# Performance work log

Hardware: AMD Instinct MI355X
Metric: run time of the kernel (lower is better)

The kernel has to match this reference:

```python
import jax, jax.numpy as jnp
import numpy as np
from jax import lax

B, C, H, W = 16, 256, 64, 64
EXP = 2
C2 = C * EXP  # expanded channels
EPS = 1e-5


def setup_inputs() -> dict:
    key = jax.random.key(0)
    ks = jax.random.split(key, 8)
    def he(k, shape, fan_out):
        return jax.random.normal(k, shape, jnp.float32) * np.sqrt(2.0 / fan_out)
    return {
        "f": jax.random.normal(ks[0], (B, C, H, W), jnp.float32),
        "ln_gamma": jnp.ones((C,), jnp.float32),
        "ln_beta": jnp.zeros((C,), jnp.float32),
        "w_expand": he(ks[1], (C2, C), C2),          # 1x1 conv [out,in]
        "freq_real": jnp.ones((C2,), jnp.float32),
        "freq_imag": jnp.zeros((C2,), jnp.float32),
        "w_poly": he(ks[2], (C2, C2), C2),
        "w_dw": he(ks[3], (C2, 1, 3, 3), 9),          # depthwise 3x3, fan_out=1*3*3
        "w_pw": he(ks[4], (C2, C2), C2),
        "w_final": he(ks[5], (C, C2), C),
    }


def reference(f, ln_gamma, ln_beta, w_expand, freq_real, freq_imag,
              w_poly, w_dw, w_pw, w_final):
    # LayerNorm over channel dim (torch permutes to NHWC, norms last dim)
    mu = jnp.mean(f, axis=1, keepdims=True)
    var = jnp.var(f, axis=1, keepdims=True)
    f1 = (f - mu) * lax.rsqrt(var + EPS)
    f1 = f1 * ln_gamma[None, :, None, None] + ln_beta[None, :, None, None]
    # 1x1 expand
    f2 = jnp.einsum('bchw,oc->bohw', f1, w_expand)
    # FFT2 -> multiply by per-channel complex scalar (r + i*j) -> IFFT2 -> real.
    # Since the filter is constant over all frequencies and f2 is real, this is
    # exactly Re((r+i*j) * f2) = r * f2; freq_imag contributes nothing.
    f4 = f2 * freq_real[None, :, None, None]
    # polymerize 1x1
    f5 = jnp.einsum('bchw,oc->bohw', f4, w_poly)
    # depthwise 3x3, SAME padding
    f6 = lax.conv_general_dilated(
        f5, w_dw, window_strides=(1, 1), padding='SAME',
        dimension_numbers=('NCHW', 'OIHW', 'NCHW'), feature_group_count=C2)
    # pointwise 1x1
    f6 = jnp.einsum('bchw,oc->bohw', f6, w_pw)
    # GELU (exact erf, torch default) gating
    f7 = jax.nn.gelu(f6, approximate=False) * f6
    # 1x1 reduce + residual
    f8 = jnp.einsum('bchw,oc->bohw', f7, w_final)
    return f + f8
```

## Files before the change

### kernel.cpp

```cpp
#include <hip/hip_runtime.h>
#include <hip/hip_bf16.h>
#include <math.h>

#define Bn 16
#define Cc 256
#define Hh 64
#define Ww 64
#define HW 4096
#define C2 512
#define Pp 65536
#define EPSc 1e-5f

typedef __attribute__((ext_vector_type(8))) short short8;
typedef __attribute__((ext_vector_type(4))) float floatx4;

__global__ __launch_bounds__(256)
void combine_weights(const float* __restrict__ w_expand,
                     const float* __restrict__ freq_real,
                     const float* __restrict__ w_poly,
                     const float* __restrict__ gamma,
                     const float* __restrict__ beta,
                     __hip_bfloat16* __restrict__ W1g_b,
                     float* __restrict__ bias1,
                     float* __restrict__ wsum) {
    int o = blockIdx.x;
    int c = threadIdx.x;
    float acc = 0.f;
    const float* wp = w_poly + (size_t)o * C2;
    for (int m = 0; m < C2; ++m) {
        acc += wp[m] * freq_real[m] * w_expand[(size_t)m * Cc + c];
    }
    float wg = acc * gamma[c];
    W1g_b[(size_t)o * Cc + c] = __float2bfloat16(wg);
    __shared__ float redB[256];
    __shared__ float redG[256];
    redB[c] = acc * beta[c];
    redG[c] = wg;
    __syncthreads();
    for (int s = 128; s > 0; s >>= 1) {
        if (c < s) { redB[c] += redB[c + s]; redG[c] += redG[c + s]; }
        __syncthreads();
    }
    if (c == 0) { bias1[o] = redB[0]; wsum[o] = redG[0]; }
}

__global__ __launch_bounds__(256)
void to_bf16(const float* __restrict__ a, __hip_bfloat16* __restrict__ o, int n) {
    int i = (blockIdx.x * 256 + threadIdx.x) * 4;
    if (i < n) {
        float4 v = *(const float4*)&a[i];
        __hip_bfloat16 r[4];
        r[0] = __float2bfloat16(v.x);
        r[1] = __float2bfloat16(v.y);
        r[2] = __float2bfloat16(v.z);
        r[3] = __float2bfloat16(v.w);
        *(uint2*)&o[i] = *(const uint2*)r;
    }
}

__global__ __launch_bounds__(256)
void pad_dw(const float* __restrict__ w_dw, float* __restrict__ w_dw_p) {
    int i = blockIdx.x * 256 + threadIdx.x;
    if (i < C2 * 12) {
        int k = i / 12, j = i - k * 12;
        w_dw_p[i] = (j < 9) ? w_dw[k * 9 + j] : 0.f;
    }
}

#define XPAD 264

__global__ __launch_bounds__(512, 4)
void gemm1f(const float* __restrict__ f,
            const __hip_bfloat16* __restrict__ W1g_b,
            const float* __restrict__ bias1,
            const float* __restrict__ wsum,
            __hip_bfloat16* __restrict__ f5) {
    __shared__ __hip_bfloat16 As[64 * XPAD];
    __shared__ float redS[32 * 64];
    __shared__ float redQ[32 * 64];
    __shared__ float muS[64];
    __shared__ float rsS[64];

    int flat = blockIdx.x;
    int b = flat >> 6;
    int h = flat & 63;
    int s0 = h * 64;

    int tid = threadIdx.x;
    int x = tid & 15;
    int cg = tid >> 4;

    const float* fb = f + (size_t)b * Cc * HW + s0 + x * 4;
    unsigned* Asu = (unsigned*)&As[0];

    float lsum[4] = {0.f, 0.f, 0.f, 0.f};
    float lsq[4]  = {0.f, 0.f, 0.f, 0.f};
#pragma unroll
    for (int i = 0; i < 4; ++i) {
        int cp = i * 32 + cg;
        float4 v0 = *(const float4*)&fb[(size_t)(cp * 2) * HW];
        float4 v1 = *(const float4*)&fb[(size_t)(cp * 2 + 1) * HW];
        float a0[4] = {v0.x, v0.y, v0.z, v0.w};
        float a1[4] = {v1.x, v1.y, v1.z, v1.w};
#pragma unroll
        for (int j = 0; j < 4; ++j) {
            lsum[j] += a0[j] + a1[j];
            lsq[j]  += a0[j] * a0[j] + a1[j] * a1[j];
            unsigned pk = ((unsigned)__bfloat16_as_ushort(__float2bfloat16(a1[j])) << 16)
                        |  (unsigned)__bfloat16_as_ushort(__float2bfloat16(a0[j]));
            Asu[(size_t)(x * 4 + j) * (XPAD / 2) + cp] = pk;
        }
    }
#pragma unroll
    for (int j = 0; j < 4; ++j) {
        redS[cg * 64 + x * 4 + j] = lsum[j];
        redQ[cg * 64 + x * 4 + j] = lsq[j];
    }

    int lane = tid & 63, wave = tid >> 6;
    int col = lane & 15, quad = lane >> 4;
    int c0w = wave * 64;
    const __hip_bfloat16* Bp = W1g_b + (size_t)(c0w + col) * Cc + quad * 8;
    short8 b_cur[4], b_nxt[4];
#pragma unroll
    for (int j = 0; j < 4; ++j)
        b_cur[j] = *(const short8*)(Bp + (size_t)j * 16 * Cc);

    __syncthreads();
    if (tid < 64) {
        float s = 0.f, q = 0.f;
#pragma unroll
        for (int g = 0; g < 32; ++g) { s += redS[g * 64 + tid]; q += redQ[g * 64 + tid]; }
        float m = s * (1.0f / 256.0f);
        muS[tid] = m;
        rsS[tid] = rsqrtf(q * (1.0f / 256.0f) - m * m + EPSc);
    }
    __syncthreads();

    floatx4 acc[4][4];
#pragma unroll
    for (int i = 0; i < 4; ++i)
#pragma unroll
        for (int j = 0; j < 4; ++j)
            acc[i][j] = (floatx4){0.f, 0.f, 0.f, 0.f};

#pragma unroll
    for (int ks = 0; ks < 8; ++ks) {
        int k0 = ks * 32;
        if (ks < 7) {
#pragma unroll
            for (int j = 0; j < 4; ++j)
                b_nxt[j] = *(const short8*)(Bp + (size_t)j * 16 * Cc + k0 + 32);
        }
        short8 af[4];
#pragma unroll
        for (int i = 0; i < 4; ++i)
            af[i] = *(const short8*)&As[(size_t)(i * 16 + col) * XPAD + k0 + quad * 8];
#pragma unroll
        for (int i = 0; i < 4; ++i)
#pragma unroll
            for (int j = 0; j < 4; ++j)
                acc[i][j] = __builtin_amdgcn_mfma_f32_16x16x32_bf16(af[i], b_cur[j], acc[i][j], 0, 0, 0);
        if (ks < 7) {
#pragma unroll
            for (int j = 0; j < 4; ++j) b_cur[j] = b_nxt[j];
        }
    }

    __hip_bfloat16* f5b = f5 + (size_t)b * C2 * HW + s0;
#pragma unroll
    for (int i = 0; i < 4; ++i) {
        int pl = i * 16 + quad * 4;
        float4 mu4 = *(const float4*)&muS[pl];
        float4 rs4 = *(const float4*)&rsS[pl];
        float mu_[4] = {mu4.x, mu4.y, mu4.z, mu4.w};
        float rs_[4] = {rs4.x, rs4.y, rs4.z, rs4.w};
#pragma unroll
        for (int j = 0; j < 4; ++j) {
            int c = c0w + j * 16 + col;
            float ws_ = wsum[c], bi_ = bias1[c];
            __hip_bfloat16 v4[4];
#pragma unroll
            for (int r = 0; r < 4; ++r) {
                float v = (acc[i][j][r] - mu_[r] * ws_) * rs_[r] + bi_;
                v4[r] = __float2bfloat16(v);
            }
            *(uint2*)&f5b[(size_t)c * HW + pl] = *(const uint2*)v4;
        }
    }
}

#define TPITCH 520

__global__ __launch_bounds__(512, 4)
void fused_tail(const __hip_bfloat16* __restrict__ f5,
                const float* __restrict__ w_dw_p,
                const __hip_bfloat16* __restrict__ w_pw_b,
                const __hip_bfloat16* __restrict__ w_final_b,
                const float* __restrict__ f,
                float* __restrict__ out) {
    __shared__ __hip_bfloat16 tT[64 * TPITCH];

    int flat = blockIdx.x;
    int xcd = flat & 7;
    int slot = flat >> 3;
    int hb = slot & 7;
    int b  = slot >> 3;
    int h  = xcd * 8 + hb;

    int tid = threadIdx.x;
    int lane = tid & 63;
    int wave = tid >> 6;
    int col = lane & 15;
    int quad = lane >> 4;

    const __hip_bfloat16* f5b = f5 + (size_t)b * C2 * HW;
    int t4 = tid & 3;
    int kb = tid >> 2;
    int w16 = t4 * 16;

    uint4 curC[3][2], nxtC[3][2];
#pragma unroll
    for (int dy = 0; dy < 3; ++dy) {
        int hh = h + dy - 1;
        if ((unsigned)hh < Hh) {
            const __hip_bfloat16* row = f5b + (size_t)kb * HW + hh * Ww + w16;
            curC[dy][0] = *(const uint4*)&row[0];
            curC[dy][1] = *(const uint4*)&row[8];
        } else {
            curC[dy][0] = make_uint4(0, 0, 0, 0);
            curC[dy][1] = make_uint4(0, 0, 0, 0);
        }
    }

#pragma unroll
    for (int it = 0; it < 4; ++it) {
        int k = it * 128 + kb;
        if (it < 3) {
            int k2 = k + 128;
#pragma unroll
            for (int dy = 0; dy < 3; ++dy) {
                int hh = h + dy - 1;
                if ((unsigned)hh < Hh) {
                    const __hip_bfloat16* row = f5b + (size_t)k2 * HW + hh * Ww + w16;
                    nxtC[dy][0] = *(const uint4*)&row[0];
                    nxtC[dy][1] = *(const uint4*)&row[8];
                } else {
                    nxtC[dy][0] = make_uint4(0, 0, 0, 0);
                    nxtC[dy][1] = make_uint4(0, 0, 0, 0);
                }
            }
        }
        const float4* wd4 = (const float4*)(w_dw_p + (size_t)k * 12);
        float4 wa = wd4[0], wb = wd4[1], wc2 = wd4[2];
        float wreg[9] = {wa.x, wa.y, wa.z, wa.w, wb.x, wb.y, wb.z, wb.w, wc2.x};
        float acc16[16] = {};
#pragma unroll
        for (int dy = 0; dy < 3; ++dy) {
            const __hip_bfloat16* pv = (const __hip_bfloat16*)&curC[dy][0];
            float cv[16];
#pragma unroll
            for (int j = 0; j < 16; ++j) cv[j] = __bfloat162float(pv[j]);
            float l_in = __shfl_up(cv[15], 1);
            float r_in = __shfl_down(cv[0], 1);
            if (t4 == 0) l_in = 0.f;
            if (t4 == 3) r_in = 0.f;
            float win[18];
            win[0] = l_in;
#pragma unroll
            for (int j = 0; j < 16; ++j) win[j + 1] = cv[j];
            win[17] = r_in;
#pragma unroll
            for (int j = 0; j < 16; ++j)
                acc16[j] += wreg[dy * 3 + 0] * win[j] +
                            wreg[dy * 3 + 1] * win[j + 1] +
                            wreg[dy * 3 + 2] * win[j + 2];
        }
#pragma unroll
        for (int j = 0; j < 16; ++j)
            tT[(size_t)(w16 + j) * TPITCH + k] = __float2bfloat16(acc16[j]);
        if (it < 3) {
#pragma unroll
            for (int dy = 0; dy < 3; ++dy) {
                curC[dy][0] = nxtC[dy][0];
                curC[dy][1] = nxtC[dy][1];
            }
        }
    }

    int wm0 = wave * 64;
    const __hip_bfloat16* Ap = w_pw_b + (size_t)(wm0 + col) * C2 + quad * 8;
    short8 a_cur[4], a_nxt[4];
#pragma unroll
    for (int mt = 0; mt < 4; ++mt)
        a_cur[mt] = *(const short8*)(Ap + (size_t)mt * 16 * C2);

    __syncthreads();

    floatx4 acc[4][4];
#pragma unroll
    for (int mt = 0; mt < 4; ++mt)
#pragma unroll
        for (int nt = 0; nt < 4; ++nt)
            acc[mt][nt] = (floatx4){0.f, 0.f, 0.f, 0.f};

#pragma unroll
    for (int ks = 0; ks < 16; ++ks) {
        int k0 = ks * 32;
        if (ks < 15) {
#pragma unroll
            for (int mt = 0; mt < 4; ++mt)
                a_nxt[mt] = *(const short8*)(Ap + (size_t)mt * 16 * C2 + k0 + 32);
        }
        short8 bfr[4];
#pragma unroll
        for (int nt = 0; nt < 4; ++nt)
            bfr[nt] = *(const short8*)&tT[(size_t)(nt * 16 + col) * TPITCH + k0 + quad * 8];
#pragma unroll
        for (int mt = 0; mt < 4; ++mt)
#pragma unroll
            for (int nt = 0; nt < 4; ++nt)
                acc[mt][nt] = __builtin_amdgcn_mfma_f32_16x16x32_bf16(a_cur[mt], bfr[nt], acc[mt][nt], 0, 0, 0);
        if (ks < 15) {
#pragma unroll
            for (int mt = 0; mt < 4; ++mt) a_cur[mt] = a_nxt[mt];
        }
    }
    __syncthreads();

#pragma unroll
    for (int mt = 0; mt < 4; ++mt)
#pragma unroll
        for (int nt = 0; nt < 4; ++nt) {
            __hip_bfloat16 v4[4];
#pragma unroll
            for (int r = 0; r < 4; ++r) {
                float v = acc[mt][nt][r];
                float gl = 0.5f * v * (1.0f + erff(v * 0.70710678118f));
                v4[r] = __float2bfloat16(gl * v);
            }
            *(uint2*)&tT[(size_t)(nt * 16 + col) * TPITCH + wm0 + mt * 16 + quad * 4] = *(const uint2*)v4;
        }

    int wm2 = wave * 32;
    const __hip_bfloat16* Af = w_final_b + (size_t)(wm2 + col) * C2 + quad * 8;
    short8 c_cur[2], c_nxt[2];
#pragma unroll
    for (int mt = 0; mt < 2; ++mt)
        c_cur[mt] = *(const short8*)(Af + (size_t)mt * 16 * C2);

    const float* fb = f + (size_t)b * Cc * HW + h * Ww;
    float* ob = out + (size_t)b * Cc * HW + h * Ww;
    float fres[2][4][4];
#pragma unroll
    for (int mt = 0; mt < 2; ++mt)
#pragma unroll
        for (int nt = 0; nt < 4; ++nt)
#pragma unroll
            for (int r = 0; r < 4; ++r) {
                int m = wm2 + mt * 16 + quad * 4 + r;
                int n = nt * 16 + col;
                fres[mt][nt][r] = fb[(size_t)m * HW + n];
            }

    __syncthreads();

    floatx4 acc2[2][4];
#pragma unroll
    for (int mt = 0; mt < 2; ++mt)
#pragma unroll
        for (int nt = 0; nt < 4; ++nt)
            acc2[mt][nt] = (floatx4){0.f, 0.f, 0.f, 0.f};

#pragma unroll
    for (int ks = 0; ks < 16; ++ks) {
        int k0 = ks * 32;
        if (ks < 15) {
#pragma unroll
            for (int mt = 0; mt < 2; ++mt)
                c_nxt[mt] = *(const short8*)(Af + (size_t)mt * 16 * C2 + k0 + 32);
        }
        short8 bfr[4];
#pragma unroll
        for (int nt = 0; nt < 4; ++nt)
            bfr[nt] = *(const short8*)&tT[(size_t)(nt * 16 + col) * TPITCH + k0 + quad * 8];
#pragma unroll
        for (int mt = 0; mt < 2; ++mt)
#pragma unroll
            for (int nt = 0; nt < 4; ++nt)
                acc2[mt][nt] = __builtin_amdgcn_mfma_f32_16x16x32_bf16(c_cur[mt], bfr[nt], acc2[mt][nt], 0, 0, 0);
        if (ks < 15) {
#pragma unroll
            for (int mt = 0; mt < 2; ++mt) c_cur[mt] = c_nxt[mt];
        }
    }

#pragma unroll
    for (int mt = 0; mt < 2; ++mt)
#pragma unroll
        for (int nt = 0; nt < 4; ++nt)
#pragma unroll
            for (int r = 0; r < 4; ++r) {
                int m = wm2 + mt * 16 + quad * 4 + r;
                int n = nt * 16 + col;
                ob[(size_t)m * HW + n] = fres[mt][nt][r] + acc2[mt][nt][r];
            }
}

extern "C" void kernel_launch(void* const* d_in, const int* in_sizes, int n_in,
                              void* d_out, int out_size, void* d_ws, size_t ws_size,
                              hipStream_t stream) {
    const float* f         = (const float*)d_in[0];
    const float* ln_gamma  = (const float*)d_in[1];
    const float* ln_beta   = (const float*)d_in[2];
    const float* w_expand  = (const float*)d_in[3];
    const float* freq_real = (const float*)d_in[4];
    const float* w_poly    = (const float*)d_in[6];
    const float* w_dw      = (const float*)d_in[7];
    const float* w_pw      = (const float*)d_in[8];
    const float* w_final   = (const float*)d_in[9];
    float* out = (float*)d_out;

    char* p = (char*)d_ws;
    __hip_bfloat16* f5   = (__hip_bfloat16*)p;  p += (size_t)C2 * Pp * 2;
    __hip_bfloat16* W1g_b = (__hip_bfloat16*)p; p += (size_t)C2 * Cc * 2;
    float* bias1 = (float*)p;                   p += (size_t)C2 * 4;
    float* wsum  = (float*)p;                   p += (size_t)C2 * 4;
    __hip_bfloat16* w_pw_b    = (__hip_bfloat16*)p;  p += (size_t)C2 * C2 * 2;
    __hip_bfloat16* w_final_b = (__hip_bfloat16*)p;  p += (size_t)Cc * C2 * 2;
    float* w_dw_p = (float*)p;                  p += (size_t)C2 * 12 * 4;

    combine_weights<<<dim3(C2), dim3(256), 0, stream>>>(
        w_expand, freq_real, w_poly, ln_gamma, ln_beta, W1g_b, bias1, wsum);

    to_bf16<<<dim3((C2 * C2 / 4 + 255) / 256), dim3(256), 0, stream>>>(
        w_pw, w_pw_b, C2 * C2);
    to_bf16<<<dim3((Cc * C2 / 4 + 255) / 256), dim3(256), 0, stream>>>(
        w_final, w_final_b, Cc * C2);
    pad_dw<<<dim3((C2 * 12 + 255) / 256), dim3(256), 0, stream>>>(w_dw, w_dw_p);

    gemm1f<<<dim3(1024), dim3(512), 0, stream>>>(
        f, W1g_b, bias1, wsum, f5);

    fused_tail<<<dim3(1024), dim3(512), 0, stream>>>(
        f5, w_dw_p, w_pw_b, w_final_b, f, out);
}
```

Before: 362.0 us.

## Deepen register prefetch, add MFMA priority hints, and fuse weight prep launches

Weight fragments in all three MFMA loops and the depthwise input rows are now double-buffered two steps ahead instead of one, with s_setprio raised around MFMA bursts. The per-channel epilogue constants in gemm1f are loaded early. The separate to_bf16 and pad_dw launches are merged into one prep kernel, and combine_weights splits its reduction over 512 threads. The aim is to hide global load latency and cut launch overhead, at the cost of extra registers that could pressure occupancy under launch_bounds(512,4).

```diff
diff --git a/kernel.cpp b/kernel.cpp
--- a/kernel.cpp
+++ b/kernel.cpp
@@ -14,7 +14,7 @@
 typedef __attribute__((ext_vector_type(8))) short short8;
 typedef __attribute__((ext_vector_type(4))) float floatx4;
 
-__global__ __launch_bounds__(256)
+__global__ __launch_bounds__(512)
 void combine_weights(const float* __restrict__ w_expand,
                      const float* __restrict__ freq_real,
                      const float* __restrict__ w_poly,
@@ -24,46 +24,65 @@
                      float* __restrict__ bias1,
                      float* __restrict__ wsum) {
     int o = blockIdx.x;
-    int c = threadIdx.x;
+    int tid = threadIdx.x;
+    int c = tid & 255;
+    int kh = tid >> 8;
     float acc = 0.f;
-    const float* wp = w_poly + (size_t)o * C2;
-    for (int m = 0; m < C2; ++m) {
-        acc += wp[m] * freq_real[m] * w_expand[(size_t)m * Cc + c];
-    }
-    float wg = acc * gamma[c];
-    W1g_b[(size_t)o * Cc + c] = __float2bfloat16(wg);
+    const float* wp = w_poly + (size_t)o * C2 + kh * 256;
+    const float* fr = freq_real + kh * 256;
+    const float* we = w_expand + (size_t)(kh * 256) * Cc + c;
+    for (int m = 0; m < 256; ++m) {
+        acc += wp[m] * fr[m] * we[(size_t)m * Cc];
+    }
+    __shared__ float part[512];
     __shared__ float redB[256];
     __shared__ float redG[256];
-    redB[c] = acc * beta[c];
-    redG[c] = wg;
+    part[tid] = acc;
+    __syncthreads();
+    if (tid < 256) {
+        float a = part[tid] + part[tid + 256];
+        float wg = a * gamma[c];
+        W1g_b[(size_t)o * Cc + c] = __float2bfloat16(wg);
+        redB[c] = a * beta[c];
+        redG[c] = wg;
+    }
     __syncthreads();
     for (int s = 128; s > 0; s >>= 1) {
-        if (c < s) { redB[c] += redB[c + s]; redG[c] += redG[c + s]; }
+        if (tid < s) { redB[tid] += redB[tid + s]; redG[tid] += redG[tid + s]; }
         __syncthreads();
     }
-    if (c == 0) { bias1[o] = redB[0]; wsum[o] = redG[0]; }
+    if (tid == 0) { bias1[o] = redB[0]; wsum[o] = redG[0]; }
+}
+
+__device__ inline void cvt4(const float* __restrict__ a,
+                            __hip_bfloat16* __restrict__ o, int q) {
+    float4 v = *(const float4*)&a[q * 4];
+    __hip_bfloat16 r[4];
+    r[0] = __float2bfloat16(v.x);
+    r[1] = __float2bfloat16(v.y);
+    r[2] = __float2bfloat16(v.z);
+    r[3] = __float2bfloat16(v.w);
+    *(uint2*)&o[q * 4] = *(const uint2*)r;
 }
 
 __global__ __launch_bounds__(256)
-void to_bf16(const float* __restrict__ a, __hip_bfloat16* __restrict__ o, int n) {
-    int i = (blockIdx.x * 256 + threadIdx.x) * 4;
-    if (i < n) {
-        float4 v = *(const float4*)&a[i];
-        __hip_bfloat16 r[4];
-        r[0] = __float2bfloat16(v.x);
-        r[1] = __float2bfloat16(v.y);
-        r[2] = __float2bfloat16(v.z);
-        r[3] = __float2bfloat16(v.w);
-        *(uint2*)&o[i] = *(const uint2*)r;
-    }
-}
-
-__global__ __launch_bounds__(256)
-void pad_dw(const float* __restrict__ w_dw, float* __restrict__ w_dw_p) {
+void prep_weights(const float* __restrict__ w_pw,
+                  const float* __restrict__ w_final,
+                  const float* __restrict__ w_dw,
+                  __hip_bfloat16* __restrict__ w_pw_b,
+                  __hip_bfloat16* __restrict__ w_final_b,
+                  float* __restrict__ w_dw_p) {
     int i = blockIdx.x * 256 + threadIdx.x;
-    if (i < C2 * 12) {
-        int k = i / 12, j = i - k * 12;
-        w_dw_p[i] = (j < 9) ? w_dw[k * 9 + j] : 0.f;
+    if (i < 65536) {
+        cvt4(w_pw, w_pw_b, i);
+    } else if (i < 98304) {
+        cvt4(w_final, w_final_b, i - 65536);
+    } else {
+        int j = i - 98304;
+        if (j < C2 * 12) {
+            int k = j / 12, l = j - k * 12;
+            w_dw_p[j] = (l < 9) ? w_dw[k * 9 + l] : 0.f;
+        }
     }
 }
 
@@ -121,10 +140,20 @@
     int col = lane & 15, quad = lane >> 4;
     int c0w = wave * 64;
     const __hip_bfloat16* Bp = W1g_b + (size_t)(c0w + col) * Cc + quad * 8;
-    short8 b_cur[4], b_nxt[4];
-#pragma unroll
-    for (int j = 0; j < 4; ++j)
-        b_cur[j] = *(const short8*)(Bp + (size_t)j * 16 * Cc);
+    short8 B0[4], B1[4];
+#pragma unroll
+    for (int j = 0; j < 4; ++j) {
+        B0[j] = *(const short8*)(Bp + (size_t)j * 16 * Cc);
+        B1[j] = *(const short8*)(Bp + (size_t)j * 16 * Cc + 32);
+    }
+
+    float ws4[4], bi4[4];
+#pragma unroll
+    for (int j = 0; j < 4; ++j) {
+        int c = c0w + j * 16 + col;
+        ws4[j] = wsum[c];
+        bi4[j] = bias1[c];
+    }
 
     __syncthreads();
     if (tid < 64) {
@@ -147,23 +176,24 @@
 #pragma unroll
     for (int ks = 0; ks < 8; ++ks) {
         int k0 = ks * 32;
-        if (ks < 7) {
-#pragma unroll
-            for (int j = 0; j < 4; ++j)
-                b_nxt[j] = *(const short8*)(Bp + (size_t)j * 16 * Cc + k0 + 32);
-        }
         short8 af[4];
 #pragma unroll
         for (int i = 0; i < 4; ++i)
             af[i] = *(const short8*)&As[(size_t)(i * 16 + col) * XPAD + k0 + quad * 8];
+        __builtin_amdgcn_s_setprio(1);
 #pragma unroll
         for (int i = 0; i < 4; ++i)
 #pragma unroll
             for (int j = 0; j < 4; ++j)
-                acc[i][j] = __builtin_amdgcn_mfma_f32_16x16x32_bf16(af[i], b_cur[j], acc[i][j], 0, 0, 0);
-        if (ks < 7) {
-#pragma unroll
-            for (int j = 0; j < 4; ++j) b_cur[j] = b_nxt[j];
+                acc[i][j] = __builtin_amdgcn_mfma_f32_16x16x32_bf16(
+                    af[i], (ks & 1) ? B1[j] : B0[j], acc[i][j], 0, 0, 0);
+        __builtin_amdgcn_s_setprio(0);
+        if (ks + 2 < 8) {
+#pragma unroll
+            for (int j = 0; j < 4; ++j) {
+                short8 v = *(const short8*)(Bp + (size_t)j * 16 * Cc + k0 + 64);
+                if (ks & 1) B1[j] = v; else B0[j] = v;
+            }
         }
     }
 
@@ -178,11 +208,10 @@
 #pragma unroll
         for (int j = 0; j < 4; ++j) {
             int c = c0w + j * 16 + col;
-            float ws_ = wsum[c], bi_ = bias1[c];
             __hip_bfloat16 v4[4];
 #pragma unroll
             for (int r = 0; r < 4; ++r) {
-                float v = (acc[i][j][r] - mu_[r] * ws_) * rs_[r] + bi_;
+                float v = (acc[i][j][r] - mu_[r] * ws4[j]) * rs_[r] + bi4[j];
                 v4[r] = __float2bfloat16(v);
             }
             *(uint2*)&f5b[(size_t)c * HW + pl] = *(const uint2*)v4;
@@ -191,6 +220,21 @@
 }
 
 #define TPITCH 520
+
+#define P0_LOAD(dst, itc) do {                                               \
+    int kk_ = (itc) * 128 + kb;                                              \
+    _Pragma("unroll")                                                        \
+    for (int dy_ = 0; dy_ < 3; ++dy_) {                                      \
+        int hh_ = h + dy_ - 1;                                               \
+        if ((unsigned)hh_ < Hh) {                                            \
+            const __hip_bfloat16* row_ = f5b + (size_t)kk_ * HW + hh_ * Ww + w16; \
+            dst[dy_][0] = *(const uint4*)&row_[0];                           \
+            dst[dy_][1] = *(const uint4*)&row_[8];                           \
+        } else {                                                             \
+            dst[dy_][0] = make_uint4(0, 0, 0, 0);                            \
+            dst[dy_][1] = make_uint4(0, 0, 0, 0);                            \
+        }                                                                    \
+    } } while (0)
 
 __global__ __launch_bounds__(512, 4)
 void fused_tail(const __hip_bfloat16* __restrict__ f5,
@@ -219,45 +263,21 @@
     int kb = tid >> 2;
     int w16 = t4 * 16;
 
-    uint4 curC[3][2], nxtC[3][2];
-#pragma unroll
-    for (int dy = 0; dy < 3; ++dy) {
-        int hh = h + dy - 1;
-        if ((unsigned)hh < Hh) {
-            const __hip_bfloat16* row = f5b + (size_t)kb * HW + hh * Ww + w16;
-            curC[dy][0] = *(const uint4*)&row[0];
-            curC[dy][1] = *(const uint4*)&row[8];
-        } else {
-            curC[dy][0] = make_uint4(0, 0, 0, 0);
-            curC[dy][1] = make_uint4(0, 0, 0, 0);
-        }
-    }
+    uint4 bA[3][2], bB[3][2];
+    P0_LOAD(bA, 0);
+    P0_LOAD(bB, 1);
 
 #pragma unroll
     for (int it = 0; it < 4; ++it) {
         int k = it * 128 + kb;
-        if (it < 3) {
-            int k2 = k + 128;
-#pragma unroll
-            for (int dy = 0; dy < 3; ++dy) {
-                int hh = h + dy - 1;
-                if ((unsigned)hh < Hh) {
-                    const __hip_bfloat16* row = f5b + (size_t)k2 * HW + hh * Ww + w16;
-                    nxtC[dy][0] = *(const uint4*)&row[0];
-                    nxtC[dy][1] = *(const uint4*)&row[8];
-                } else {
-                    nxtC[dy][0] = make_uint4(0, 0, 0, 0);
-                    nxtC[dy][1] = make_uint4(0, 0, 0, 0);
-                }
-            }
-        }
         const float4* wd4 = (const float4*)(w_dw_p + (size_t)k * 12);
         float4 wa = wd4[0], wb = wd4[1], wc2 = wd4[2];
         float wreg[9] = {wa.x, wa.y, wa.z, wa.w, wb.x, wb.y, wb.z, wb.w, wc2.x};
         float acc16[16] = {};
 #pragma unroll
         for (int dy = 0; dy < 3; ++dy) {
-            const __hip_bfloat16* pv = (const __hip_bfloat16*)&curC[dy][0];
+            const __hip_bfloat16* pv =
+                (const __hip_bfloat16*)((it & 1) ? &bB[dy][0] : &bA[dy][0]);
             float cv[16];
 #pragma unroll
             for (int j = 0; j < 16; ++j) cv[j] = __bfloat162float(pv[j]);
@@ -276,26 +296,26 @@
                             wreg[dy * 3 + 1] * win[j + 1] +
                             wreg[dy * 3 + 2] * win[j + 2];
         }
+        if (it + 2 < 4) {
+            if (it & 1) { P0_LOAD(bB, it + 2); } else { P0_LOAD(bA, it + 2); }
+        }
 #pragma unroll
         for (int j = 0; j < 16; ++j)
             tT[(size_t)(w16 + j) * TPITCH + k] = __float2bfloat16(acc16[j]);
-        if (it < 3) {
-#pragma unroll
-            for (int dy = 0; dy < 3; ++dy) {
-                curC[dy][0] = nxtC[dy][0];
-                curC[dy][1] = nxtC[dy][1];
-            }
-        }
     }
 
     int wm0 = wave * 64;
     const __hip_bfloat16* Ap = w_pw_b + (size_t)(wm0 + col) * C2 + quad * 8;
-    short8 a_cur[4], a_nxt[4];
+    short8 A0[4], A1[4];
 #pragma unroll
     for (int mt = 0; mt < 4; ++mt)
-        a_cur[mt] = *(const short8*)(Ap + (size_t)mt * 16 * C2);
-
-    __syncthreads();
+        A0[mt] = *(const short8*)(Ap + (size_t)mt * 16 * C2);
+
+    __syncthreads();
+
+#pragma unroll
+    for (int mt = 0; mt < 4; ++mt)
+        A1[mt] = *(const short8*)(Ap + (size_t)mt * 16 * C2 + 32);
 
     floatx4 acc[4][4];
 #pragma unroll
@@ -307,23 +327,24 @@
 #pragma unroll
     for (int ks = 0; ks < 16; ++ks) {
         int k0 = ks * 32;
-        if (ks < 15) {
-#pragma unroll
-            for (int mt = 0; mt < 4; ++mt)
-                a_nxt[mt] = *(const short8*)(Ap + (size_t)mt * 16 * C2 + k0 + 32);
-        }
         short8 bfr[4];
 #pragma unroll
         for (int nt = 0; nt < 4; ++nt)
             bfr[nt] = *(const short8*)&tT[(size_t)(nt * 16 + col) * TPITCH + k0 + quad * 8];
+        __builtin_amdgcn_s_setprio(1);
 #pragma unroll
         for (int mt = 0; mt < 4; ++mt)
 #pragma unroll
             for (int nt = 0; nt < 4; ++nt)
-                acc[mt][nt] = __builtin_amdgcn_mfma_f32_16x16x32_bf16(a_cur[mt], bfr[nt], acc[mt][nt], 0, 0, 0);
-        if (ks < 15) {
-#pragma unroll
-            for (int mt = 0; mt < 4; ++mt) a_cur[mt] = a_nxt[mt];
+                acc[mt][nt] = __builtin_amdgcn_mfma_f32_16x16x32_bf16(
+                    (ks & 1) ? A1[mt] : A0[mt], bfr[nt], acc[mt][nt], 0, 0, 0);
+        __builtin_amdgcn_s_setprio(0);
+        if (ks + 2 < 16) {
+#pragma unroll
+            for (int mt = 0; mt < 4; ++mt) {
+                short8 v = *(const short8*)(Ap + (size_t)mt * 16 * C2 + k0 + 64);
+                if (ks & 1) A1[mt] = v; else A0[mt] = v;
+            }
         }
     }
     __syncthreads();
@@ -344,10 +365,10 @@
 
     int wm2 = wave * 32;
     const __hip_bfloat16* Af = w_final_b + (size_t)(wm2 + col) * C2 + quad * 8;
-    short8 c_cur[2], c_nxt[2];
+    short8 C0[2], C1[2];
 #pragma unroll
     for (int mt = 0; mt < 2; ++mt)
-        c_cur[mt] = *(const short8*)(Af + (size_t)mt * 16 * C2);
+        C0[mt] = *(const short8*)(Af + (size_t)mt * 16 * C2);
 
     const float* fb = f + (size_t)b * Cc * HW + h * Ww;
     float* ob = out + (size_t)b * Cc * HW + h * Ww;
@@ -365,6 +386,10 @@
 
     __syncthreads();
 
+#pragma unroll
+    for (int mt = 0; mt < 2; ++mt)
+        C1[mt] = *(const short8*)(Af + (size_t)mt * 16 * C2 + 32);
+
     floatx4 acc2[2][4];
 #pragma unroll
     for (int mt = 0; mt < 2; ++mt)
@@ -375,23 +400,24 @@
 #pragma unroll
     for (int ks = 0; ks < 16; ++ks) {
         int k0 = ks * 32;
-        if (ks < 15) {
-#pragma unroll
-            for (int mt = 0; mt < 2; ++mt)
-                c_nxt[mt] = *(const short8*)(Af + (size_t)mt * 16 * C2 + k0 + 32);
-        }
         short8 bfr[4];
 #pragma unroll
         for (int nt = 0; nt < 4; ++nt)
             bfr[nt] = *(const short8*)&tT[(size_t)(nt * 16 + col) * TPITCH + k0 + quad * 8];
+        __builtin_amdgcn_s_setprio(1);
 #pragma unroll
         for (int mt = 0; mt < 2; ++mt)
 #pragma unroll
             for (int nt = 0; nt < 4; ++nt)
-                acc2[mt][nt] = __builtin_amdgcn_mfma_f32_16x16x32_bf16(c_cur[mt], bfr[nt], acc2[mt][nt], 0, 0, 0);
-        if (ks < 15) {
-#pragma unroll
-            for (int mt = 0; mt < 2; ++mt) c_cur[mt] = c_nxt[mt];
+                acc2[mt][nt] = __builtin_amdgcn_mfma_f32_16x16x32_bf16(
+                    (ks & 1) ? C1[mt] : C0[mt], bfr[nt], acc2[mt][nt], 0, 0, 0);
+        __builtin_amdgcn_s_setprio(0);
+        if (ks + 2 < 16) {
+#pragma unroll
+            for (int mt = 0; mt < 2; ++mt) {
+                short8 v = *(const short8*)(Af + (size_t)mt * 16 * C2 + k0 + 64);
+                if (ks & 1) C1[mt] = v; else C0[mt] = v;
+            }
         }
     }
 
@@ -430,14 +456,11 @@
     __hip_bfloat16* w_final_b = (__hip_bfloat16*)p;  p += (size_t)Cc * C2 * 2;
     float* w_dw_p = (float*)p;                  p += (size_t)C2 * 12 * 4;
 
-    combine_weights<<<dim3(C2), dim3(256), 0, stream>>>(
+    combine_weights<<<dim3(C2), dim3(512), 0, stream>>>(
         w_expand, freq_real, w_poly, ln_gamma, ln_beta, W1g_b, bias1, wsum);
 
-    to_bf16<<<dim3((C2 * C2 / 4 + 255) / 256), dim3(256), 0, stream>>>(
-        w_pw, w_pw_b, C2 * C2);
-    to_bf16<<<dim3((Cc * C2 / 4 + 255) / 256), dim3(256), 0, stream>>>(
-        w_final, w_final_b, Cc * C2);
-    pad_dw<<<dim3((C2 * 12 + 255) / 256), dim3(256), 0, stream>>>(w_dw, w_dw_p);
+    prep_weights<<<dim3(409), dim3(256), 0, stream>>>(
+        w_pw, w_final, w_dw, w_pw_b, w_final_b, w_dw_p);
 
     gemm1f<<<dim3(1024), dim3(512), 0, stream>>>(
         f, W1g_b, bias1, wsum, f5);
```

Result: faster. 343.4 us (-5.1%).
